# Performance work log

Measured on AMD Instinct MI355X. Metric: run time of the kernel, lower is better.

## Reference

```python
import jax, jax.numpy as jnp
import numpy as np

N_E = 1024
E_DIM = 64
BETA = 0.4
N_TOK = 131072


def setup_inputs() -> dict:
    key = jax.random.key(0)
    k1, k2 = jax.random.split(key)
    z = jax.random.normal(k1, (N_TOK, E_DIM), dtype=jnp.float32)
    # torch init: uniform(-1/n_e, 1/n_e)
    codebook = jax.random.uniform(k2, (N_E, E_DIM), dtype=jnp.float32,
                                  minval=-1.0 / N_E, maxval=1.0 / N_E)
    return {"z": z, "codebook": codebook}


def reference(z, codebook):
    sg = jax.lax.stop_gradient
    # squared euclidean distances: [N, n_e]
    d = (jnp.sum(z * z, axis=1, keepdims=True)
         + jnp.sum(codebook * codebook, axis=1)
         - 2.0 * jnp.matmul(z, codebook.T))
    idx = jnp.argmin(d, axis=1)                      # [N]
    z_q = codebook[idx]                              # gather, [N, E_DIM]
    # commitment / codebook loss
    vq_loss = (jnp.mean((sg(z_q) - z) ** 2)
               + BETA * jnp.mean((z_q - sg(z)) ** 2))
    # straight-through estimator
    z_q_st = z + sg(z_q - z)
    # codebook usage statistics (mean of one-hot encodings)
    e_mean = jnp.bincount(idx, length=N_E).astype(z.dtype) / jnp.asarray(idx.shape[0], z.dtype)
    usage_loss = -jnp.sum(e_mean * jnp.log(e_mean + 1e-10))
    perplexity = jnp.exp(usage_loss)
    vq_loss = vq_loss + 0.01 * usage_loss
    return z_q_st, vq_loss, idx[:, None], perplexity
```

## Files before the change

kernel.cpp:

```cpp
#include <hip/hip_runtime.h>
#include <math.h>

#define N_TOK 131072
#define N_E   1024
#define E_DIM 64
#define BETA  0.4

#define ZQ_OFF   0
#define LOSS_OFF 8388608
#define IDX_OFF  8388609
#define PERP_OFF 8519681

#define WS_C2    0
#define WS_CNT   4096
#define WS_SSQ   8192
#define WS_WLC   8200
#define WS_FHI   8208
#define WS_FLO   139280
#define WS_WL    270352
#define WS_KEYS  303120
#define WLCAP    8192

typedef short bf16x8 __attribute__((ext_vector_type(8)));
typedef float f32x4  __attribute__((ext_vector_type(4)));
typedef unsigned long long u64;

__device__ __forceinline__ unsigned short f32_to_bf16_rn(float f) {
    unsigned u = __float_as_uint(f);
    unsigned r = (u + 0x7fffu + ((u >> 16) & 1u)) >> 16;
    return (unsigned short)r;
}
__device__ __forceinline__ float bf16_to_f32(unsigned short h) {
    return __uint_as_float(((unsigned)h) << 16);
}
__device__ __forceinline__ void gl2lds16(const void* g, void* l) {
    __builtin_amdgcn_global_load_lds(
        (const __attribute__((address_space(1))) unsigned int*)g,
        (__attribute__((address_space(3))) unsigned int*)l, 16, 0, 0);
}

__global__ void c2_kernel(const float* __restrict__ cb, float* __restrict__ c2,
                          int* __restrict__ counts, int* __restrict__ wlc,
                          double* __restrict__ sum_sq) {
    int e = blockIdx.x * blockDim.x + threadIdx.x;
    if (e < N_E) {
        const float* p = cb + (size_t)e * E_DIM;
        double s = 0.0;
#pragma unroll
        for (int k = 0; k < E_DIM; ++k) {
            double c = (double)p[k];
            s = fma(c, c, s);
        }
        c2[e] = (float)s;
        counts[e] = 0;
        if (e == 0) { *wlc = 0; *sum_sq = 0.0; }
    }
}

__global__ void frag_kernel(const float* __restrict__ cb,
                            unsigned short* __restrict__ fhi,
                            unsigned short* __restrict__ flo,
                            u64* __restrict__ keys) {
    int tid = blockIdx.x * 256 + threadIdx.x;
    if (tid < WLCAP) keys[tid] = ~0ull;
    int j  = tid & 7;
    int l  = (tid >> 3) & 63;
    int cc = tid >> 9;
    int code = (cc >> 1) * 16 + (l & 15);
    int k    = (cc & 1) * 32 + (l >> 4) * 8 + j;
    float f = cb[(size_t)code * E_DIM + k];
    unsigned short h = f32_to_bf16_rn(f);
    unsigned short lo = f32_to_bf16_rn(f - bf16_to_f32(h));
    fhi[tid] = h;
    flo[tid] = lo;
}

__device__ __attribute__((noinline)) int exact_best_serial(
    const float* __restrict__ z, const float* __restrict__ cb,
    const float* __restrict__ c2, int n) {
    const float* zr = z + (size_t)n * E_DIM;
    float r[8];
#pragma unroll
    for (int j = 0; j < 8; ++j) r[j] = __fmul_rn(zr[j], zr[j]);
#pragma unroll 1
    for (int i = 8; i < 64; i += 8)
#pragma unroll
        for (int j = 0; j < 8; ++j)
            r[j] = __fadd_rn(r[j], __fmul_rn(zr[i + j], zr[i + j]));
    float z2 = __fadd_rn(__fadd_rn(__fadd_rn(r[0], r[1]), __fadd_rn(r[2], r[3])),
                         __fadd_rn(__fadd_rn(r[4], r[5]), __fadd_rn(r[6], r[7])));
    u64 bestkey = ~0ull;
#pragma unroll 1
    for (int e = 0; e < N_E; ++e) {
        const float* cp = cb + (size_t)e * E_DIM;
        double m = 0.0;
#pragma unroll 1
        for (int i = 0; i < E_DIM; ++i)
            m = fma((double)zr[i], (double)cp[i], m);
        float d = __fsub_rn(__fadd_rn(z2, c2[e]), __fmul_rn(2.0f, (float)m));
        u64 key = ((u64)__float_as_uint(d) << 32) | (unsigned)e;
        if (key < bestkey) bestkey = key;
    }
    return (int)(bestkey & 0xffffffffu);
}

__global__ __launch_bounds__(256, 4) void vq_main(
    const float* __restrict__ z, const float* __restrict__ cb,
    const float* __restrict__ c2, const unsigned short* __restrict__ fhi_,
    const unsigned short* __restrict__ flo_, int* __restrict__ counts,
    double* __restrict__ sum_sq, int* __restrict__ wl_count,
    int* __restrict__ wl, float margin_u, float* __restrict__ out) {

    __shared__ unsigned char stagebuf[2][16384];
    __shared__ float c2s[N_E];
    __shared__ int   best_s[128];
    __shared__ unsigned char flag_s[128];
    __shared__ double wred[4];

    const int tid  = threadIdx.x;
    const int lane = tid & 63;
    const int wid  = tid >> 6;
    const int col  = lane & 15;
    const int quad = lane >> 4;
    const int blk_tok0 = blockIdx.x * 128;
    const int wave_tok0 = blk_tok0 + wid * 32;

#pragma unroll
    for (int i = 0; i < 4; ++i)
        c2s[tid * 4 + i] = fmaf(-0.5f, c2[tid * 4 + i], 0.25f);

    bf16x8 Ah[2][2], Al[2][2];
#pragma unroll
    for (int m = 0; m < 2; ++m) {
        const float* zr = z + (size_t)(wave_tok0 + m * 16 + col) * E_DIM + quad * 8;
#pragma unroll
        for (int kc = 0; kc < 2; ++kc) {
            float4 u0 = *(const float4*)(zr + kc * 32);
            float4 u1 = *(const float4*)(zr + kc * 32 + 4);
            float f[8] = {u0.x, u0.y, u0.z, u0.w, u1.x, u1.y, u1.z, u1.w};
            union { unsigned short u[8]; bf16x8 v; } h, lo;
#pragma unroll
            for (int j = 0; j < 8; ++j) {
                h.u[j]  = f32_to_bf16_rn(f[j]);
                lo.u[j] = f32_to_bf16_rn(f[j] - bf16_to_f32(h.u[j]));
            }
            Ah[m][kc] = h.v;
            Al[m][kc] = lo.v;
        }
    }

    unsigned k1[2][4], k2[2][4];
#pragma unroll
    for (int m = 0; m < 2; ++m)
#pragma unroll
        for (int r = 0; r < 4; ++r) { k1[m][r] = 0u; k2[m][r] = 0u; }

    const char* hsrc0 = (const char*)fhi_;
    const char* lsrc0 = (const char*)flo_;
    auto stage = [&](int s, int b) {
#pragma unroll
        for (int i = 0; i < 2; ++i) {
            gl2lds16(hsrc0 + s * 8192 + i * 4096 + tid * 16,
                     &stagebuf[b][i * 4096 + wid * 1024]);
            gl2lds16(lsrc0 + s * 8192 + i * 4096 + tid * 16,
                     &stagebuf[b][8192 + i * 4096 + wid * 1024]);
        }
    };

    const f32x4 zero4 = {0.f, 0.f, 0.f, 0.f};
    stage(0, 0);
    for (int s = 0; s < 16; ++s) {
        __syncthreads();
        if (s + 1 < 16) stage(s + 1, (s + 1) & 1);
        const unsigned char* hb = &stagebuf[s & 1][0];
        const unsigned char* lb = &stagebuf[s & 1][8192];
#pragma unroll
        for (int cl = 0; cl < 4; ++cl) {
            const int c = s * 4 + cl;
            const int off0 = (cl * 2) * 1024 + lane * 16;
            union { uint4 u; bf16x8 v; } bh0, bh1, bl0, bl1;
            bh0.u = *(const uint4*)(hb + off0);
            bh1.u = *(const uint4*)(hb + off0 + 1024);
            bl0.u = *(const uint4*)(lb + off0);
            bl1.u = *(const uint4*)(lb + off0 + 1024);
            const float ch = c2s[c * 16 + col];
            const f32x4 cinit = {ch, ch, ch, ch};
            const unsigned ctag = (unsigned)(63 - c);
#pragma unroll
            for (int m = 0; m < 2; ++m) {
                f32x4 acc1 = __builtin_amdgcn_mfma_f32_16x16x32_bf16(Ah[m][0], bh0.v, cinit, 0, 0, 0);
                f32x4 acc2 = __builtin_amdgcn_mfma_f32_16x16x32_bf16(Ah[m][1], bh1.v, zero4, 0, 0, 0);
                acc1 = __builtin_amdgcn_mfma_f32_16x16x32_bf16(Ah[m][0], bl0.v, acc1, 0, 0, 0);
                acc2 = __builtin_amdgcn_mfma_f32_16x16x32_bf16(Ah[m][1], bl1.v, acc2, 0, 0, 0);
                acc1 = __builtin_amdgcn_mfma_f32_16x16x32_bf16(Al[m][0], bh0.v, acc1, 0, 0, 0);
                acc2 = __builtin_amdgcn_mfma_f32_16x16x32_bf16(Al[m][1], bh1.v, acc2, 0, 0, 0);
#pragma unroll
                for (int r = 0; r < 4; ++r) {
                    float u = acc1[r] + acc2[r];
                    unsigned key = (__float_as_uint(u) & 0xFFFFFFC0u) | ctag;
                    unsigned hi2 = min(k1[m][r], key);
                    k2[m][r] = max(k2[m][r], hi2);
                    k1[m][r] = max(k1[m][r], key);
                }
            }
        }
    }

#pragma unroll
    for (int m = 0; m < 2; ++m) {
#pragma unroll
        for (int r = 0; r < 4; ++r) {
            float v1 = __uint_as_float(k1[m][r] & 0xFFFFFFC0u);
            float v2 = __uint_as_float(k2[m][r] & 0xFFFFFFC0u);
            int   b1 = (63 - (int)(k1[m][r] & 63u)) * 16 + col;
#pragma unroll
            for (int d = 1; d < 16; d <<= 1) {
                float o1 = __shfl_xor(v1, d, 64);
                float o2 = __shfl_xor(v2, d, 64);
                int   ob = __shfl_xor(b1, d, 64);
                float n2 = fmaxf(fmaxf(v2, o2), fminf(v1, o1));
                bool take = (o1 > v1) || (o1 == v1 && ob < b1);
                v1 = fmaxf(v1, o1);
                b1 = take ? ob : b1;
                v2 = n2;
            }
            if (col == 0) {
                int tl = wid * 32 + m * 16 + quad * 4 + r;
                int n  = blk_tok0 + tl;
                int best = b1;
                bool fl = (v1 - v2) < margin_u;
                if (fl) {
                    int pos = atomicAdd(wl_count, 1);
                    if (pos < WLCAP) wl[pos] = n;
                    else { best = exact_best_serial(z, cb, c2, n); fl = false; }
                }
                best_s[tl] = best;
                flag_s[tl] = fl ? 1 : 0;
                if (!fl) atomicAdd(&counts[best], 1);
            }
        }
    }
    __syncthreads();

    if (tid < 128) out[IDX_OFF + blk_tok0 + tid] = (float)best_s[tid];

    const int sub = tid & 15, grp = tid >> 4;
    double dl = 0.0;
    const float4* zrow = (const float4*)z;
    const float4* crow = (const float4*)cb;
    float4* qrow = (float4*)(out + ZQ_OFF);
#pragma unroll
    for (int p = 0; p < 8; ++p) {
        int tl = p * 16 + grp;
        if (!flag_s[tl]) {
            int n = blk_tok0 + tl;
            float4 z4 = zrow[(size_t)n * 16 + sub];
            float4 c4 = crow[(size_t)best_s[tl] * 16 + sub];
            float dx = c4.x - z4.x, dy = c4.y - z4.y;
            float dz = c4.z - z4.z, dw = c4.w - z4.w;
            float4 q;
            q.x = z4.x + dx; q.y = z4.y + dy;
            q.z = z4.z + dz; q.w = z4.w + dw;
            qrow[(size_t)n * 16 + sub] = q;
            dl += (double)dx * dx + (double)dy * dy
                + (double)dz * dz + (double)dw * dw;
        }
    }
#pragma unroll
    for (int off = 32; off > 0; off >>= 1)
        dl += __shfl_down(dl, off, 64);
    if (lane == 0) wred[wid] = dl;
    __syncthreads();
    if (tid == 0)
        atomicAdd(sum_sq, wred[0] + wred[1] + wred[2] + wred[3]);
}

__global__ __launch_bounds__(64) void fixup_scan(
    const float* __restrict__ z, const float* __restrict__ cb,
    const float* __restrict__ c2, const int* __restrict__ wl,
    const int* __restrict__ wl_count, u64* __restrict__ keys) {

    int count = *wl_count; if (count > WLCAP) count = WLCAP;
    const int g = blockIdx.x >> 5;
    const int s = blockIdx.x & 31;
    if (g * 64 >= count) return;
    const int lane = threadIdx.x;
    const int w = g * 64 + lane;
    const bool valid = w < count;
    const int n = wl[valid ? w : g * 64];

    double zd[E_DIM];
    const float4* zp = (const float4*)(z + (size_t)n * E_DIM);
#pragma unroll
    for (int k = 0; k < 16; ++k) {
        float4 v = zp[k];
        zd[4 * k]     = (double)v.x;
        zd[4 * k + 1] = (double)v.y;
        zd[4 * k + 2] = (double)v.z;
        zd[4 * k + 3] = (double)v.w;
    }
    float r8[8];
#pragma unroll
    for (int j = 0; j < 8; ++j) {
        float f = (float)zd[j];
        r8[j] = __fmul_rn(f, f);
    }
#pragma unroll
    for (int i = 8; i < 64; i += 8)
#pragma unroll
        for (int j = 0; j < 8; ++j) {
            float f = (float)zd[i + j];
            r8[j] = __fadd_rn(r8[j], __fmul_rn(f, f));
        }
    const float z2 = __fadd_rn(
        __fadd_rn(__fadd_rn(r8[0], r8[1]), __fadd_rn(r8[2], r8[3])),
        __fadd_rn(__fadd_rn(r8[4], r8[5]), __fadd_rn(r8[6], r8[7])));

    u64 best = ~0ull;
    const int e0 = s * 32;
    for (int e = e0; e < e0 + 32; ++e) {
        const float* cp = cb + (size_t)e * E_DIM;
        double m = 0.0;
#pragma unroll
        for (int i = 0; i < E_DIM; ++i)
            m = fma(zd[i], (double)cp[i], m);
        float d = __fsub_rn(__fadd_rn(z2, c2[e]), __fmul_rn(2.0f, (float)m));
        u64 key = ((u64)__float_as_uint(d) << 32) | (unsigned)e;
        if (key < best) best = key;
    }
    if (valid) atomicMin(&keys[w], best);
}

__global__ __launch_bounds__(256) void fixup_apply(
    const float* __restrict__ z, const float* __restrict__ cb,
    const int* __restrict__ wl, const int* __restrict__ wl_count,
    const u64* __restrict__ keys, int* __restrict__ counts,
    double* __restrict__ sum_sq, float* __restrict__ out) {

    int count = *wl_count; if (count > WLCAP) count = WLCAP;
    const int lane = threadIdx.x & 63;
    const int gw = blockIdx.x * 4 + (threadIdx.x >> 6);
    for (int w = gw; w < count; w += 1024) {
        const int n = wl[w];
        const int best = (int)(keys[w] & 0xffffffffull);
        float cv = cb[(size_t)best * E_DIM + lane];
        float zi = z[(size_t)n * E_DIM + lane];
        float diff = cv - zi;
        out[ZQ_OFF + (size_t)n * E_DIM + lane] = zi + diff;
        double d2 = (double)diff * (double)diff;
#pragma unroll
        for (int off = 32; off > 0; off >>= 1)
            d2 += __shfl_down(d2, off, 64);
        if (lane == 0) {
            atomicAdd(sum_sq, d2);
            atomicAdd(&counts[best], 1);
            out[IDX_OFF + n] = (float)best;
        }
    }
}

__global__ __launch_bounds__(1024) void finalize_kernel(
    const int* __restrict__ counts, const double* __restrict__ sum_sq,
    float* __restrict__ out) {
    __shared__ double red[1024];
    int e = threadIdx.x;
    double em = (double)counts[e] / (double)N_TOK;
    red[e] = -em * log(em + 1e-10);
    __syncthreads();
    for (int s = 512; s > 0; s >>= 1) {
        if (e < s) red[e] += red[e + s];
        __syncthreads();
    }
    if (e == 0) {
        double usage = red[0];
        double mse = sum_sq[0] / (double)((size_t)N_TOK * E_DIM);
        out[LOSS_OFF] = (float)((1.0 + BETA) * mse + 0.01 * usage);
        out[PERP_OFF] = (float)exp(usage);
    }
}

extern "C" void kernel_launch(void* const* d_in, const int* in_sizes, int n_in,
                              void* d_out, int out_size, void* d_ws, size_t ws_size,
                              hipStream_t stream) {
    const float* z  = (const float*)d_in[0];
    const float* cb = (const float*)d_in[1];
    float* out = (float*)d_out;

    float*          c2     = (float*)((char*)d_ws + WS_C2);
    int*            counts = (int*)((char*)d_ws + WS_CNT);
    double*         sum_sq = (double*)((char*)d_ws + WS_SSQ);
    int*            wlc    = (int*)((char*)d_ws + WS_WLC);
    unsigned short* fhi    = (unsigned short*)((char*)d_ws + WS_FHI);
    unsigned short* flo    = (unsigned short*)((char*)d_ws + WS_FLO);
    int*            wl     = (int*)((char*)d_ws + WS_WL);
    u64*            keys   = (u64*)((char*)d_ws + WS_KEYS);

    float margin_u = (ws_size >= (size_t)(WS_KEYS + 8 * WLCAP)) ? 2.25e-5f : 0.0f;

    c2_kernel<<<4, 256, 0, stream>>>(cb, c2, counts, wlc, sum_sq);
    frag_kernel<<<256, 256, 0, stream>>>(cb, fhi, flo, keys);
    vq_main<<<1024, 256, 0, stream>>>(z, cb, c2, fhi, flo, counts, sum_sq,
                                      wlc, wl, margin_u, out);
    fixup_scan<<<4096, 64, 0, stream>>>(z, cb, c2, wl, wlc, keys);
    fixup_apply<<<256, 256, 0, stream>>>(z, cb, wl, wlc, keys, counts,
                                         sum_sq, out);
    finalize_kernel<<<1, 1024, 0, stream>>>(counts, sum_sq, out);
}
```

Baseline: 219.1 us.

## Replace split-bf16 triple MFMA with single scaled fp16 MFMA and wider fixup margin

Switches the distance GEMM from a three-term bf16 hi/lo split to a single fp16 MFMA pass, with the codebook prescaled by 1024 so its fp16 values keep precision and the c2 bias scaled to match. The low-part fragment buffer goes away, which halves staged codebook traffic and cuts MFMAs per tile from six to two. It also merges the c2 kernel into the fragment kernel, removing one launch. In exchange the candidate margin is widened and the worklist capacity and fixup grid are doubled, so more tokens may need the exact fp64 rescan.

Result: slower. 311.8 us (+42.3%).

```diff
diff --git a/kernel.cpp b/kernel.cpp
--- a/kernel.cpp
+++ b/kernel.cpp
@@ -15,64 +15,50 @@
 #define WS_CNT   4096
 #define WS_SSQ   8192
 #define WS_WLC   8200
-#define WS_FHI   8208
-#define WS_FLO   139280
-#define WS_WL    270352
-#define WS_KEYS  303120
-#define WLCAP    8192
-
-typedef short bf16x8 __attribute__((ext_vector_type(8)));
+#define WS_FH    8208
+#define WS_WL    139280
+#define WS_KEYS  204816
+#define WLCAP    16384
+
+typedef _Float16 f16x8 __attribute__((ext_vector_type(8)));
 typedef float f32x4  __attribute__((ext_vector_type(4)));
 typedef unsigned long long u64;
 
-__device__ __forceinline__ unsigned short f32_to_bf16_rn(float f) {
-    unsigned u = __float_as_uint(f);
-    unsigned r = (u + 0x7fffu + ((u >> 16) & 1u)) >> 16;
-    return (unsigned short)r;
-}
-__device__ __forceinline__ float bf16_to_f32(unsigned short h) {
-    return __uint_as_float(((unsigned)h) << 16);
-}
 __device__ __forceinline__ void gl2lds16(const void* g, void* l) {
     __builtin_amdgcn_global_load_lds(
         (const __attribute__((address_space(1))) unsigned int*)g,
         (__attribute__((address_space(3))) unsigned int*)l, 16, 0, 0);
 }
 
-__global__ void c2_kernel(const float* __restrict__ cb, float* __restrict__ c2,
-                          int* __restrict__ counts, int* __restrict__ wlc,
-                          double* __restrict__ sum_sq) {
-    int e = blockIdx.x * blockDim.x + threadIdx.x;
-    if (e < N_E) {
-        const float* p = cb + (size_t)e * E_DIM;
+__global__ void frag_kernel(const float* __restrict__ cb,
+                            unsigned short* __restrict__ fh,
+                            u64* __restrict__ keys,
+                            float* __restrict__ c2,
+                            int* __restrict__ counts, int* __restrict__ wlc,
+                            double* __restrict__ sum_sq) {
+    int tid = blockIdx.x * 256 + threadIdx.x;
+    if (tid < WLCAP) keys[tid] = ~0ull;
+    if (tid < N_E) {
+        const float* p = cb + (size_t)tid * E_DIM;
         double s = 0.0;
 #pragma unroll
         for (int k = 0; k < E_DIM; ++k) {
             double c = (double)p[k];
             s = fma(c, c, s);
         }
-        c2[e] = (float)s;
-        counts[e] = 0;
-        if (e == 0) { *wlc = 0; *sum_sq = 0.0; }
-    }
-}
-
-__global__ void frag_kernel(const float* __restrict__ cb,
-                            unsigned short* __restrict__ fhi,
-                            unsigned short* __restrict__ flo,
-                            u64* __restrict__ keys) {
-    int tid = blockIdx.x * 256 + threadIdx.x;
-    if (tid < WLCAP) keys[tid] = ~0ull;
+        c2[tid] = (float)s;
+        counts[tid] = 0;
+        if (tid == 0) { *wlc = 0; *sum_sq = 0.0; }
+    }
     int j  = tid & 7;
     int l  = (tid >> 3) & 63;
     int cc = tid >> 9;
     int code = (cc >> 1) * 16 + (l & 15);
     int k    = (cc & 1) * 32 + (l >> 4) * 8 + j;
-    float f = cb[(size_t)code * E_DIM + k];
-    unsigned short h = f32_to_bf16_rn(f);
-    unsigned short lo = f32_to_bf16_rn(f - bf16_to_f32(h));
-    fhi[tid] = h;
-    flo[tid] = lo;
+    float f = cb[(size_t)code * E_DIM + k] * 1024.0f;
+    union { _Float16 h; unsigned short s; } cv;
+    cv.h = (_Float16)f;
+    fh[tid] = cv.s;
 }
 
 __device__ __attribute__((noinline)) int exact_best_serial(
@@ -106,10 +92,10 @@
 
 __global__ __launch_bounds__(256, 4) void vq_main(
     const float* __restrict__ z, const float* __restrict__ cb,
-    const float* __restrict__ c2, const unsigned short* __restrict__ fhi_,
-    const unsigned short* __restrict__ flo_, int* __restrict__ counts,
-    double* __restrict__ sum_sq, int* __restrict__ wl_count,
-    int* __restrict__ wl, float margin_u, float* __restrict__ out) {
+    const float* __restrict__ c2, const unsigned short* __restrict__ fh_,
+    int* __restrict__ counts, double* __restrict__ sum_sq,
+    int* __restrict__ wl_count, int* __restrict__ wl, float margin_u,
+    float* __restrict__ out) {
 
     __shared__ unsigned char stagebuf[2][16384];
     __shared__ float c2s[N_E];
@@ -125,11 +111,21 @@
     const int blk_tok0 = blockIdx.x * 128;
     const int wave_tok0 = blk_tok0 + wid * 32;
 
+    const char* hsrc0 = (const char*)fh_;
+    auto stage = [&](int s, int b) {
+#pragma unroll
+        for (int i = 0; i < 4; ++i)
+            gl2lds16(hsrc0 + s * 16384 + i * 4096 + tid * 16,
+                     &stagebuf[b][i * 4096 + wid * 1024]);
+    };
+
+    stage(0, 0);
+
 #pragma unroll
     for (int i = 0; i < 4; ++i)
-        c2s[tid * 4 + i] = fmaf(-0.5f, c2[tid * 4 + i], 0.25f);
-
-    bf16x8 Ah[2][2], Al[2][2];
+        c2s[tid * 4 + i] = fmaf(-512.0f, c2[tid * 4 + i], 64.0f);
+
+    f16x8 Ah[2][2];
 #pragma unroll
     for (int m = 0; m < 2; ++m) {
         const float* zr = z + (size_t)(wave_tok0 + m * 16 + col) * E_DIM + quad * 8;
@@ -137,15 +133,12 @@
         for (int kc = 0; kc < 2; ++kc) {
             float4 u0 = *(const float4*)(zr + kc * 32);
             float4 u1 = *(const float4*)(zr + kc * 32 + 4);
-            float f[8] = {u0.x, u0.y, u0.z, u0.w, u1.x, u1.y, u1.z, u1.w};
-            union { unsigned short u[8]; bf16x8 v; } h, lo;
-#pragma unroll
-            for (int j = 0; j < 8; ++j) {
-                h.u[j]  = f32_to_bf16_rn(f[j]);
-                lo.u[j] = f32_to_bf16_rn(f[j] - bf16_to_f32(h.u[j]));
-            }
-            Ah[m][kc] = h.v;
-            Al[m][kc] = lo.v;
+            f16x8 a;
+            a[0] = (_Float16)u0.x; a[1] = (_Float16)u0.y;
+            a[2] = (_Float16)u0.z; a[3] = (_Float16)u0.w;
+            a[4] = (_Float16)u1.x; a[5] = (_Float16)u1.y;
+            a[6] = (_Float16)u1.z; a[7] = (_Float16)u1.w;
+            Ah[m][kc] = a;
         }
     }
 
@@ -155,49 +148,29 @@
 #pragma unroll
         for (int r = 0; r < 4; ++r) { k1[m][r] = 0u; k2[m][r] = 0u; }
 
-    const char* hsrc0 = (const char*)fhi_;
-    const char* lsrc0 = (const char*)flo_;
-    auto stage = [&](int s, int b) {
-#pragma unroll
-        for (int i = 0; i < 2; ++i) {
-            gl2lds16(hsrc0 + s * 8192 + i * 4096 + tid * 16,
-                     &stagebuf[b][i * 4096 + wid * 1024]);
-            gl2lds16(lsrc0 + s * 8192 + i * 4096 + tid * 16,
-                     &stagebuf[b][8192 + i * 4096 + wid * 1024]);
-        }
-    };
-
-    const f32x4 zero4 = {0.f, 0.f, 0.f, 0.f};
-    stage(0, 0);
-    for (int s = 0; s < 16; ++s) {
+    for (int s = 0; s < 8; ++s) {
         __syncthreads();
-        if (s + 1 < 16) stage(s + 1, (s + 1) & 1);
+        if (s + 1 < 8) stage(s + 1, (s + 1) & 1);
         const unsigned char* hb = &stagebuf[s & 1][0];
-        const unsigned char* lb = &stagebuf[s & 1][8192];
-#pragma unroll
-        for (int cl = 0; cl < 4; ++cl) {
-            const int c = s * 4 + cl;
-            const int off0 = (cl * 2) * 1024 + lane * 16;
-            union { uint4 u; bf16x8 v; } bh0, bh1, bl0, bl1;
-            bh0.u = *(const uint4*)(hb + off0);
-            bh1.u = *(const uint4*)(hb + off0 + 1024);
-            bl0.u = *(const uint4*)(lb + off0);
-            bl1.u = *(const uint4*)(lb + off0 + 1024);
+#pragma unroll
+        for (int cl = 0; cl < 8; ++cl) {
+            const int c = s * 8 + cl;
+            const int off0 = cl * 2048 + lane * 16;
+            union { uint4 u; f16x8 v; } b0, b1;
+            b0.u = *(const uint4*)(hb + off0);
+            b1.u = *(const uint4*)(hb + off0 + 1024);
             const float ch = c2s[c * 16 + col];
             const f32x4 cinit = {ch, ch, ch, ch};
             const unsigned ctag = (unsigned)(63 - c);
 #pragma unroll
             for (int m = 0; m < 2; ++m) {
-                f32x4 acc1 = __builtin_amdgcn_mfma_f32_16x16x32_bf16(Ah[m][0], bh0.v, cinit, 0, 0, 0);
-                f32x4 acc2 = __builtin_amdgcn_mfma_f32_16x16x32_bf16(Ah[m][1], bh1.v, zero4, 0, 0, 0);
-                acc1 = __builtin_amdgcn_mfma_f32_16x16x32_bf16(Ah[m][0], bl0.v, acc1, 0, 0, 0);
-                acc2 = __builtin_amdgcn_mfma_f32_16x16x32_bf16(Ah[m][1], bl1.v, acc2, 0, 0, 0);
-                acc1 = __builtin_amdgcn_mfma_f32_16x16x32_bf16(Al[m][0], bh0.v, acc1, 0, 0, 0);
-                acc2 = __builtin_amdgcn_mfma_f32_16x16x32_bf16(Al[m][1], bh1.v, acc2, 0, 0, 0);
+                f32x4 acc = __builtin_amdgcn_mfma_f32_16x16x32_f16(
+                    Ah[m][0], b0.v, cinit, 0, 0, 0);
+                acc = __builtin_amdgcn_mfma_f32_16x16x32_f16(
+                    Ah[m][1], b1.v, acc, 0, 0, 0);
 #pragma unroll
                 for (int r = 0; r < 4; ++r) {
-                    float u = acc1[r] + acc2[r];
-                    unsigned key = (__float_as_uint(u) & 0xFFFFFFC0u) | ctag;
+                    unsigned key = (__float_as_uint(acc[r]) & 0xFFFFFFC0u) | ctag;
                     unsigned hi2 = min(k1[m][r], key);
                     k2[m][r] = max(k2[m][r], hi2);
                     k1[m][r] = max(k1[m][r], key);
@@ -390,18 +363,16 @@
     int*            counts = (int*)((char*)d_ws + WS_CNT);
     double*         sum_sq = (double*)((char*)d_ws + WS_SSQ);
     int*            wlc    = (int*)((char*)d_ws + WS_WLC);
-    unsigned short* fhi    = (unsigned short*)((char*)d_ws + WS_FHI);
-    unsigned short* flo    = (unsigned short*)((char*)d_ws + WS_FLO);
+    unsigned short* fh     = (unsigned short*)((char*)d_ws + WS_FH);
     int*            wl     = (int*)((char*)d_ws + WS_WL);
     u64*            keys   = (u64*)((char*)d_ws + WS_KEYS);
 
-    float margin_u = (ws_size >= (size_t)(WS_KEYS + 8 * WLCAP)) ? 2.25e-5f : 0.0f;
-
-    c2_kernel<<<4, 256, 0, stream>>>(cb, c2, counts, wlc, sum_sq);
-    frag_kernel<<<256, 256, 0, stream>>>(cb, fhi, flo, keys);
-    vq_main<<<1024, 256, 0, stream>>>(z, cb, c2, fhi, flo, counts, sum_sq,
+    float margin_u = (ws_size >= (size_t)(WS_KEYS + 8 * WLCAP)) ? 0.07f : 0.0f;
+
+    frag_kernel<<<256, 256, 0, stream>>>(cb, fh, keys, c2, counts, wlc, sum_sq);
+    vq_main<<<1024, 256, 0, stream>>>(z, cb, c2, fh, counts, sum_sq,
                                       wlc, wl, margin_u, out);
-    fixup_scan<<<4096, 64, 0, stream>>>(z, cb, c2, wl, wlc, keys);
+    fixup_scan<<<8192, 64, 0, stream>>>(z, cb, c2, wl, wlc, keys);
     fixup_apply<<<256, 256, 0, stream>>>(z, cb, wl, wlc, keys, counts,
                                          sum_sq, out);
     finalize_kernel<<<1, 1024, 0, stream>>>(counts, sum_sq, out);
```
